# Kernel tuning notes

Measured on AMD Instinct MI355X. Metric: run time of the kernel, lower is better.

Reference implementation:

```python
import jax, jax.numpy as jnp
import numpy as np

NEG_SLOPE = 0.2  # PyG GATConv default


def gat_conv(x, src, dst, W, att_src, att_dst, bias, num_nodes, concat):
    """Faithful PyG GATConv forward (self-loops assumed already added).
    x: [N, F_in]; src/dst: [E]; W: [F_in, H*C]; att_src/att_dst: [H, C]."""
    H, C = att_src.shape
    h = (x @ W).reshape(num_nodes, H, C)                      # [N, H, C]
    a_src = (h * att_src[None]).sum(-1)                       # [N, H]
    a_dst = (h * att_dst[None]).sum(-1)                       # [N, H]
    alpha = jax.nn.leaky_relu(a_src[src] + a_dst[dst], NEG_SLOPE)  # [E, H]
    # segment softmax over incoming edges of each dst node (numerically stable)
    m = jax.ops.segment_max(alpha, dst, num_segments=num_nodes)    # [N, H]
    e = jnp.exp(alpha - m[dst])                                    # [E, H]
    denom = jax.ops.segment_sum(e, dst, num_segments=num_nodes)    # [N, H]
    w = e / jnp.maximum(denom[dst], 1e-16)                         # [E, H]
    msg = h[src] * w[:, :, None]                                   # [E, H, C]
    out = jax.ops.segment_sum(msg, dst, num_segments=num_nodes)    # [N, H, C]
    out = out.reshape(num_nodes, H * C) if concat else out.mean(axis=1)
    return out + bias


def setup_inputs() -> dict:
    key = jax.random.key(0)
    ks = jax.random.split(key, 16)
    N, E, n_drones = 100000, 1600000, 10000
    IN, HID, OUT, HEADS = 6, 64, 2, 4

    x = jax.random.normal(ks[0], (N, IN), dtype=jnp.float32)
    # first n_drones nodes are drones (x[:,5] == 1.0), rest 0.0
    x = x.at[:, 5].set((jnp.arange(N) < n_drones).astype(jnp.float32))
    edge_index = jax.random.randint(ks[1], (2, E), 0, N, dtype=jnp.int64)

    s = 0.1
    params = {
        "W1": jax.random.normal(ks[2], (IN, HEADS * HID), jnp.float32) * s,
        "att_src1": jax.random.normal(ks[3], (HEADS, HID), jnp.float32) * s,
        "att_dst1": jax.random.normal(ks[4], (HEADS, HID), jnp.float32) * s,
        "b1": jax.random.normal(ks[5], (HEADS * HID,), jnp.float32) * s,
        "W2": jax.random.normal(ks[6], (HEADS * HID, HID), jnp.float32) * s,
        "att_src2": jax.random.normal(ks[7], (1, HID), jnp.float32) * s,
        "att_dst2": jax.random.normal(ks[8], (1, HID), jnp.float32) * s,
        "b2": jax.random.normal(ks[9], (HID,), jnp.float32) * s,
        "fc1_w": jax.random.normal(ks[10], (HID, 64), jnp.float32) * s,
        "fc1_b": jax.random.normal(ks[11], (64,), jnp.float32) * s,
        "fc2_w": jax.random.normal(ks[12], (64, OUT), jnp.float32) * s,
        "fc2_b": jax.random.normal(ks[13], (OUT,), jnp.float32) * s,
    }
    return {"x": x, "edge_index": edge_index, "n_drones": n_drones, **params}


def reference(x, edge_index, n_drones, W1, att_src1, att_dst1, b1,
              W2, att_src2, att_dst2, b2, fc1_w, fc1_b, fc2_w, fc2_b):
    N = x.shape[0]
    action_scale = 2.0
    # add self loops (PyG GATConv default add_self_loops=True)
    loop = jnp.arange(N, dtype=edge_index.dtype)
    src = jnp.concatenate([edge_index[0], loop])
    dst = jnp.concatenate([edge_index[1], loop])

    h = jax.nn.elu(gat_conv(x, src, dst, W1, att_src1, att_dst1, b1, N, concat=True))
    h = jax.nn.elu(gat_conv(h, src, dst, W2, att_src2, att_dst2, b2, N, concat=False))

    drone_idx = jnp.nonzero(x[:, 5] == 1.0, size=n_drones)[0]
    h_drones = h[drone_idx]                                   # [n_drones, HID]
    out = jnp.tanh(jax.nn.relu(h_drones @ fc1_w + fc1_b) @ fc2_w + fc2_b)
    return out * action_scale
```

## Files before the change

### kernel.cpp

```cpp
#include <hip/hip_runtime.h>
#include <hip/hip_fp16.h>
#include <math.h>

#define CAP 48
#define PARTBITS 8
#define BINW 256
#define NB 240
#define SEGCAP 48

typedef float f32x4 __attribute__((ext_vector_type(4)));
typedef __bf16 bf16x8 __attribute__((ext_vector_type(8)));
typedef unsigned short ushort8 __attribute__((ext_vector_type(8)));
typedef int i32x4 __attribute__((ext_vector_type(4)));
typedef int i32x2 __attribute__((ext_vector_type(2)));

__device__ __forceinline__ float leaky(float x){ return x > 0.f ? x : 0.2f * x; }
__device__ __forceinline__ float eluf(float x){ return x > 0.f ? x : __expf(x) - 1.f; }
__device__ __forceinline__ unsigned short f2bf(float f){
  unsigned u = __float_as_uint(f);
  u += 0x7FFF + ((u >> 16) & 1);
  return (unsigned short)(u >> 16);
}
__device__ __forceinline__ float bf2f(unsigned short u){
  return __uint_as_float(((unsigned)u) << 16);
}
__device__ __forceinline__ unsigned short f2h(float f){
  return __half_as_ushort(__float2half(f));
}
__device__ __forceinline__ float h2f(unsigned short u){
  return __half2float(__ushort_as_half(u));
}

__global__ __launch_bounds__(256) void k1_att1(const float* __restrict__ x,
    const float* __restrict__ W1, const float* __restrict__ as1,
    const float* __restrict__ ad1, const float* __restrict__ W2,
    unsigned short* __restrict__ Bfrag, ushort8* __restrict__ rec8,
    int* __restrict__ gtail, int N){
  __shared__ float vw[48];
  int t = threadIdx.x;
  int gid = blockIdx.x * 256 + t;
  if (gid == 0) *gtail = 0;
  if (gid < 16384){
    int j  = gid & 7;
    int L  = (gid >> 3) & 63;
    int ct = (gid >> 9) & 3;
    int ks = gid >> 11;
    int k = ks*32 + ((L >> 4) & 3)*8 + j;
    int c = ct*16 + (L & 15);
    Bfrag[gid] = f2bf(W2[k*64 + c]);
  }
  if (t < 48){
    int side = t / 24, r = t % 24, f = r / 4, h = r % 4;
    const float* att = side ? ad1 : as1;
    float s = 0.f;
    for (int c = 0; c < 64; ++c) s += W1[f*256 + h*64 + c] * att[h*64 + c];
    vw[side*24 + f*4 + h] = s;
  }
  __syncthreads();
  int n = gid;
  if (n >= N) return;
  float xf[6];
  for (int f = 0; f < 6; ++f) xf[f] = x[n*6 + f];
  float as[4], ad[4];
  for (int h = 0; h < 4; ++h){
    float s = 0.f, d = 0.f;
    for (int f = 0; f < 6; ++f){ s += xf[f] * vw[f*4 + h]; d += xf[f] * vw[24 + f*4 + h]; }
    as[h] = s; ad[h] = d;
  }
  ushort8 v0, v1;
  v0[0]=f2bf(xf[0]); v0[1]=f2bf(xf[1]); v0[2]=f2bf(xf[2]); v0[3]=f2bf(xf[3]);
  v0[4]=f2bf(xf[4]); v0[5]=f2bf(xf[5]); v0[6]=f2h(as[0]); v0[7]=f2h(as[1]);
  v1[0]=f2h(as[2]); v1[1]=f2h(as[3]); v1[2]=f2h(ad[0]); v1[3]=f2h(ad[1]);
  v1[4]=f2h(ad[2]); v1[5]=f2h(ad[3]); v1[6]=0; v1[7]=0;
  rec8[n*2 + 0] = v0;
  rec8[n*2 + 1] = v1;
}

__global__ __launch_bounds__(256) void k2a_route(const int* __restrict__ ei,
    int E, int NR, i32x2* __restrict__ queue, int* __restrict__ qcnt){
  __shared__ int lcnt[512];
  int t = threadIdx.x, blk = blockIdx.x;
  for (int i = t; i < NR; i += 256) lcnt[i] = 0;
  __syncthreads();
  int E4 = E >> 2;
  const i32x4* s4 = (const i32x4*)ei;
  const i32x4* d4 = (const i32x4*)(ei + E);
  for (int i = blk*256 + t; i < E4; i += NB*256){
    i32x4 s = __builtin_nontemporal_load(s4 + i);
    i32x4 d = __builtin_nontemporal_load(d4 + i);
    #pragma unroll
    for (int j = 0; j < 4; ++j){
      int p = d[j] >> PARTBITS;
      int r = atomicAdd(&lcnt[p], 1);
      if (r < SEGCAP){ i32x2 v = {d[j], s[j]}; queue[((size_t)p*NB + blk)*SEGCAP + r] = v; }
    }
  }
  if (blk == 0 && t < (E & 3)){
    int e = E4*4 + t;
    int dd = ei[E + e], ss = ei[e];
    int p = dd >> PARTBITS;
    int r = atomicAdd(&lcnt[p], 1);
    if (r < SEGCAP){ i32x2 v = {dd, ss}; queue[((size_t)p*NB + blk)*SEGCAP + r] = v; }
  }
  __syncthreads();
  for (int i = t; i < NR; i += 256) qcnt[(size_t)i*NB + blk] = lcnt[i];
}

__global__ __launch_bounds__(1024) void k2b_build(const i32x2* __restrict__ queue,
    const int* __restrict__ qcnt, int* __restrict__ cnt,
    int* __restrict__ row_start, int* __restrict__ bucket,
    int* __restrict__ gtail){
  __shared__ int lc[BINW];
  __shared__ int lq[NB];
  __shared__ int spref[NB];
  __shared__ int npref[BINW+1];
  __shared__ int scan[BINW];
  __shared__ int lbuck[BINW*CAP];
  __shared__ int gbase_s;
  int t = threadIdx.x, bin = blockIdx.x;
  if (t < BINW) lc[t] = 0;
  for (int i = t; i < NB; i += 1024) lq[i] = min(qcnt[(size_t)bin*NB + i], SEGCAP);
  __syncthreads();
  if (t < 256) scan[t] = (t < NB) ? lq[t] : 0;
  __syncthreads();
  for (int off = 1; off < 256; off <<= 1){
    int v = 0;
    if (t < 256 && t >= off) v = scan[t - off];
    __syncthreads();
    if (t < 256) scan[t] += v;
    __syncthreads();
  }
  if (t < NB) spref[t] = (t == 0) ? 0 : scan[t-1];
  int V = scan[NB-1];
  __syncthreads();
  const i32x2* q = queue + (size_t)bin*NB*SEGCAP;
  for (int vi = t; vi < V; vi += 1024){
    int lo = 0, hi = NB-1;
    while (lo < hi){ int mid = (lo+hi+1) >> 1; if (spref[mid] <= vi) lo = mid; else hi = mid-1; }
    i32x2 pr = q[lo*SEGCAP + (vi - spref[lo])];
    int ld = pr.x & (BINW-1);
    int pos = atomicAdd(&lc[ld], 1);
    if (pos < CAP) lbuck[ld*CAP + pos] = pr.y;
  }
  __syncthreads();
  if (t < 256) scan[t] = min(lc[t], CAP);
  __syncthreads();
  for (int off = 1; off < 256; off <<= 1){
    int v = 0;
    if (t < 256 && t >= off) v = scan[t - off];
    __syncthreads();
    if (t < 256) scan[t] += v;
    __syncthreads();
  }
  if (t < 256) npref[t] = (t == 0) ? 0 : scan[t-1];
  if (t == 0){
    npref[BINW] = scan[BINW-1];
    gbase_s = atomicAdd(gtail, scan[BINW-1]);
  }
  __syncthreads();
  int gbase = gbase_s;
  int Vn = npref[BINW];
  for (int vi = t; vi < Vn; vi += 1024){
    int lo = 0, hi = BINW-1;
    while (lo < hi){ int mid = (lo+hi+1) >> 1; if (npref[mid] <= vi) lo = mid; else hi = mid-1; }
    bucket[gbase + vi] = lbuck[lo*CAP + (vi - npref[lo])];
  }
  if (t < BINW){
    cnt[bin*BINW + t] = min(lc[t], CAP);
    row_start[bin*BINW + t] = gbase + npref[t];
  }
}

__global__ __launch_bounds__(256) void k3_agg1(const ushort8* __restrict__ rec8,
    const int* __restrict__ cnt, const int* __restrict__ row_start,
    const int* __restrict__ bucket, float* __restrict__ aggr, int N){
  int n = blockIdx.x * 256 + threadIdx.x;
  if (n >= N) return;
  ushort8 v0 = rec8[n*2+0], v1 = rec8[n*2+1];
  float xf[6] = {bf2f(v0[0]), bf2f(v0[1]), bf2f(v0[2]), bf2f(v0[3]), bf2f(v0[4]), bf2f(v0[5])};
  float as[4] = {h2f(v0[6]), h2f(v0[7]), h2f(v1[0]), h2f(v1[1])};
  float ad[4] = {h2f(v1[2]), h2f(v1[3]), h2f(v1[4]), h2f(v1[5])};
  float acc[4][6], den[4];
  for (int h = 0; h < 4; ++h){
    float e0 = __expf(leaky(as[h] + ad[h]));
    den[h] = e0;
    for (int f = 0; f < 6; ++f) acc[h][f] = e0 * xf[f];
  }
  int deg = cnt[n];
  const int* bk = bucket + row_start[n];
  int i = 0;
  for (; i + 4 <= deg; i += 4){
    int sid[4];
    #pragma unroll
    for (int j = 0; j < 4; ++j) sid[j] = bk[i+j];
    ushort8 ra[4], rb[4];
    #pragma unroll
    for (int j = 0; j < 4; ++j){
      ra[j] = rec8[sid[j]*2+0]; rb[j] = rec8[sid[j]*2+1];
    }
    #pragma unroll
    for (int j = 0; j < 4; ++j){
      float sx[6] = {bf2f(ra[j][0]), bf2f(ra[j][1]), bf2f(ra[j][2]),
                     bf2f(ra[j][3]), bf2f(ra[j][4]), bf2f(ra[j][5])};
      float sa[4] = {h2f(ra[j][6]), h2f(ra[j][7]), h2f(rb[j][0]), h2f(rb[j][1])};
      #pragma unroll
      for (int h = 0; h < 4; ++h){
        float e = __expf(leaky(sa[h] + ad[h]));
        den[h] += e;
        #pragma unroll
        for (int f = 0; f < 6; ++f) acc[h][f] += e * sx[f];
      }
    }
  }
  for (; i < deg; ++i){
    int s = bk[i];
    ushort8 a0 = rec8[s*2+0], a1 = rec8[s*2+1];
    float sx[6] = {bf2f(a0[0]), bf2f(a0[1]), bf2f(a0[2]), bf2f(a0[3]), bf2f(a0[4]), bf2f(a0[5])};
    float sa[4] = {h2f(a0[6]), h2f(a0[7]), h2f(a1[0]), h2f(a1[1])};
    for (int h = 0; h < 4; ++h){
      float e = __expf(leaky(sa[h] + ad[h]));
      den[h] += e;
      for (int f = 0; f < 6; ++f) acc[h][f] += e * sx[f];
    }
  }
  float4* o = (float4*)(aggr + (size_t)n*32);
  o[0] = make_float4(acc[0][0], acc[0][1], acc[0][2], acc[0][3]);
  o[1] = make_float4(acc[0][4], acc[0][5], acc[1][0], acc[1][1]);
  o[2] = make_float4(acc[1][2], acc[1][3], acc[1][4], acc[1][5]);
  o[3] = make_float4(acc[2][0], acc[2][1], acc[2][2], acc[2][3]);
  o[4] = make_float4(acc[2][4], acc[2][5], acc[3][0], acc[3][1]);
  o[5] = make_float4(acc[3][2], acc[3][3], acc[3][4], acc[3][5]);
  o[6] = make_float4(den[0], den[1], den[2], den[3]);
}

__global__ __launch_bounds__(256) void k4_mfma(
    const float* __restrict__ aggr, const float* __restrict__ W1,
    const float* __restrict__ b1, const unsigned short* __restrict__ Bfrag,
    const float* __restrict__ as2v, const float* __restrict__ ad2v,
    unsigned short* __restrict__ h2h, float2* __restrict__ a2, int N){
  __shared__ float w1s[6*256];
  __shared__ float b1s[256];
  __shared__ ushort8 bfs[2048];
  int t = threadIdx.x;
  {
    const float4* w1g = (const float4*)W1;
    float4* w1l = (float4*)w1s;
    for (int i = t; i < 384; i += 256) w1l[i] = w1g[i];
    if (t < 64) ((float4*)b1s)[t] = ((const float4*)b1)[t];
    const ushort8* bfg = (const ushort8*)Bfrag;
    #pragma unroll
    for (int i = 0; i < 8; ++i) bfs[t + 256*i] = bfg[t + 256*i];
  }
  int L = t & 63;
  int w = t >> 6;
  int base = blockIdx.x * 64;
  int m = L & 15;
  int quad = L >> 4;
  int na = base + w*16 + m;
  int nc = min(na, N-1);
  const float4* A4 = (const float4*)(aggr + (size_t)nc*32);
  float4 q0=A4[0], q1=A4[1], q2=A4[2], q3=A4[3], q4=A4[4], q5=A4[5], q6=A4[6];
  float d0=1.f/q6.x, d1=1.f/q6.y, d2=1.f/q6.z, d3=1.f/q6.w;
  float af[24];
  af[0]=q0.x*d0;  af[1]=q0.y*d0;  af[2]=q0.z*d0;  af[3]=q0.w*d0;  af[4]=q1.x*d0;  af[5]=q1.y*d0;
  af[6]=q1.z*d1;  af[7]=q1.w*d1;  af[8]=q2.x*d1;  af[9]=q2.y*d1;  af[10]=q2.z*d1; af[11]=q2.w*d1;
  af[12]=q3.x*d2; af[13]=q3.y*d2; af[14]=q3.z*d2; af[15]=q3.w*d2; af[16]=q4.x*d2; af[17]=q4.y*d2;
  af[18]=q4.z*d3; af[19]=q4.w*d3; af[20]=q5.x*d3; af[21]=q5.y*d3; af[22]=q5.z*d3; af[23]=q5.w*d3;

  f32x4 acc[4];
  #pragma unroll
  for (int ct = 0; ct < 4; ++ct) acc[ct] = (f32x4){0.f, 0.f, 0.f, 0.f};
  __syncthreads();

  #pragma unroll
  for (int ks = 0; ks < 8; ++ks){
    int kb = ks*32 + quad*8;
    int kc = kb >> 6;
    const float* afk = af + kc*6;
    float4 bb0 = *(const float4*)(b1s + kb);
    float4 bb1 = *(const float4*)(b1s + kb + 4);
    float s0=bb0.x, s1=bb0.y, s2=bb0.z, s3=bb0.w;
    float s4=bb1.x, s5=bb1.y, s6=bb1.z, s7=bb1.w;
    #pragma unroll
    for (int f = 0; f < 6; ++f){
      float a = afk[f];
      float4 w0 = *(const float4*)(w1s + f*256 + kb);
      float4 w1 = *(const float4*)(w1s + f*256 + kb + 4);
      s0 += a*w0.x; s1 += a*w0.y; s2 += a*w0.z; s3 += a*w0.w;
      s4 += a*w1.x; s5 += a*w1.y; s6 += a*w1.z; s7 += a*w1.w;
    }
    ushort8 ap;
    ap[0]=f2bf(eluf(s0)); ap[1]=f2bf(eluf(s1)); ap[2]=f2bf(eluf(s2)); ap[3]=f2bf(eluf(s3));
    ap[4]=f2bf(eluf(s4)); ap[5]=f2bf(eluf(s5)); ap[6]=f2bf(eluf(s6)); ap[7]=f2bf(eluf(s7));
    bf16x8 av = __builtin_bit_cast(bf16x8, ap);
    #pragma unroll
    for (int ct = 0; ct < 4; ++ct){
      bf16x8 bv = __builtin_bit_cast(bf16x8, bfs[(ks*4 + ct)*64 + L]);
      acc[ct] = __builtin_amdgcn_mfma_f32_16x16x32_bf16(av, bv, acc[ct], 0, 0, 0);
    }
  }

  float asv[4], adv[4];
  #pragma unroll
  for (int ct = 0; ct < 4; ++ct){ asv[ct] = as2v[ct*16 + m]; adv[ct] = ad2v[ct*16 + m]; }
  float ps[4] = {0,0,0,0}, pd[4] = {0,0,0,0};
  #pragma unroll
  for (int ct = 0; ct < 4; ++ct)
    #pragma unroll
    for (int r = 0; r < 4; ++r){
      ps[r] += acc[ct][r] * asv[ct];
      pd[r] += acc[ct][r] * adv[ct];
    }
  #pragma unroll
  for (int r = 0; r < 4; ++r){
    int nr = base + w*16 + quad*4 + r;
    if (nr < N){
      #pragma unroll
      for (int ct = 0; ct < 4; ++ct)
        h2h[(size_t)nr*64 + ct*16 + m] = f2h(acc[ct][r]);
    }
  }
  #pragma unroll
  for (int mask = 1; mask <= 8; mask <<= 1){
    #pragma unroll
    for (int r = 0; r < 4; ++r){
      ps[r] += __shfl_xor(ps[r], mask, 64);
      pd[r] += __shfl_xor(pd[r], mask, 64);
    }
  }
  if (m == 0){
    #pragma unroll
    for (int r = 0; r < 4; ++r){
      int nr = base + w*16 + quad*4 + r;
      if (nr < N) a2[nr] = make_float2(ps[r], pd[r]);
    }
  }
}

__global__ __launch_bounds__(256) void k5_out(
    const unsigned short* __restrict__ h2h, const float2* __restrict__ a2,
    const int* __restrict__ cnt, const int* __restrict__ row_start,
    const int* __restrict__ bucket, const float* __restrict__ b2,
    const float* __restrict__ fc1w, const float* __restrict__ fc1b,
    const float* __restrict__ fc2w, const float* __restrict__ fc2b,
    float* __restrict__ out, int ND){
  __shared__ float hb[4][64];
  int lane = threadIdx.x & 63;
  int w = threadIdx.x >> 6;
  int n = blockIdx.x * 4 + w;
  if (n >= ND) return;
  float2 self = a2[n];
  float adv = self.y;
  float e0 = __expf(leaky(self.x + adv));
  float den = e0;
  float acc = e0 * h2f(h2h[(size_t)n*64 + lane]);
  int deg = cnt[n];
  const int* bk = bucket + row_start[n];
  int i = 0;
  for (; i + 4 <= deg; i += 4){
    int sid[4];
    #pragma unroll
    for (int j = 0; j < 4; ++j) sid[j] = bk[i+j];
    float av[4]; unsigned short hv4[4];
    #pragma unroll
    for (int j = 0; j < 4; ++j){
      av[j] = a2[sid[j]].x;
      hv4[j] = h2h[(size_t)sid[j]*64 + lane];
    }
    #pragma unroll
    for (int j = 0; j < 4; ++j){
      float e = __expf(leaky(av[j] + adv));
      den += e;
      acc += e * h2f(hv4[j]);
    }
  }
  for (; i < deg; ++i){
    int s = bk[i];
    float e = __expf(leaky(a2[s].x + adv));
    den += e;
    acc += e * h2f(h2h[(size_t)s*64 + lane]);
  }
  float hv = eluf(acc / den + b2[lane]);
  hb[w][lane] = hv;
  float t1 = fc1b[lane];
  for (int k = 0; k < 64; ++k) t1 += hb[w][k] * fc1w[k*64 + lane];
  t1 = fmaxf(t1, 0.f);
  float p0 = t1 * fc2w[lane*2 + 0];
  float p1 = t1 * fc2w[lane*2 + 1];
  for (int o = 32; o > 0; o >>= 1){
    p0 += __shfl_down(p0, o, 64);
    p1 += __shfl_down(p1, o, 64);
  }
  if (lane == 0){
    out[n*2 + 0] = tanhf(p0 + fc2b[0]) * 2.f;
    out[n*2 + 1] = tanhf(p1 + fc2b[1]) * 2.f;
  }
}

extern "C" void kernel_launch(void* const* d_in, const int* in_sizes, int n_in,
                              void* d_out, int out_size, void* d_ws, size_t ws_size,
                              hipStream_t stream){
  const float* x    = (const float*)d_in[0];
  const int*   ei   = (const int*)d_in[1];
  const float* W1   = (const float*)d_in[3];
  const float* as1  = (const float*)d_in[4];
  const float* ad1  = (const float*)d_in[5];
  const float* b1   = (const float*)d_in[6];
  const float* W2   = (const float*)d_in[7];
  const float* as2  = (const float*)d_in[8];
  const float* ad2  = (const float*)d_in[9];
  const float* b2   = (const float*)d_in[10];
  const float* fc1w = (const float*)d_in[11];
  const float* fc1b = (const float*)d_in[12];
  const float* fc2w = (const float*)d_in[13];
  const float* fc2b = (const float*)d_in[14];
  float* out = (float*)d_out;

  int N  = in_sizes[0] / 6;
  int E  = in_sizes[1] / 2;
  int ND = out_size / 2;
  int NR = (N + BINW - 1) >> PARTBITS;

  char* p = (char*)d_ws;
  auto alloc = [&](size_t bytes){ void* r = (void*)p; p += (bytes + 255) & ~(size_t)255; return r; };
  int*            cnt    = (int*)           alloc((size_t)NR * BINW * 4);
  int*            rowst  = (int*)           alloc((size_t)NR * BINW * 4);
  int*            bucket = (int*)           alloc(((size_t)E + 1024) * 4);
  ushort8*        rec8   = (ushort8*)       alloc((size_t)N * 32);
  float*          aggr   = (float*)         alloc((size_t)N * 128);
  unsigned short* h2h    = (unsigned short*)alloc((size_t)N * 128);
  float2*         a2     = (float2*)        alloc((size_t)N * 8);
  unsigned short* Bfrag  = (unsigned short*)alloc(16384 * 2);
  i32x2*          queue  = (i32x2*)         alloc((size_t)NR * NB * SEGCAP * 8);
  int*            qcnt   = (int*)           alloc((size_t)NR * NB * 4);
  int*            gtail  = (int*)           alloc(256);

  size_t needed = (size_t)(p - (char*)d_ws);
  if (needed > ws_size) return;

  k1_att1<<<(N + 255)/256, 256, 0, stream>>>(x, W1, as1, ad1, W2, Bfrag, rec8, gtail, N);
  k2a_route<<<NB, 256, 0, stream>>>(ei, E, NR, queue, qcnt);
  k2b_build<<<NR, 1024, 0, stream>>>(queue, qcnt, cnt, rowst, bucket, gtail);
  k3_agg1<<<(N + 255)/256, 256, 0, stream>>>(rec8, cnt, rowst, bucket, aggr, N);
  k4_mfma<<<(N + 63)/64, 256, 0, stream>>>(aggr, W1, b1, Bfrag, as2, ad2, h2h, a2, N);
  k5_out<<<(ND + 3)/4, 256, 0, stream>>>(h2h, a2, cnt, rowst, bucket, b2,
                                         fc1w, fc1b, fc2w, fc2b, out, ND);
}
```

Baseline: 194.4 us.

## Fuse route with att1, split layer-1 aggregation per head pair, fp16 normalized output

Merges the node-attention kernel and the edge-routing kernel into one launch, with a block-index split so both run concurrently. Layer-1 aggregation now uses two threads per node, each handling two heads. Each thread reads a 16-byte per-head-pair record (features plus two source scores) rather than a 32-byte record, and destination scores move to a separate small array. The aggregation normalizes by the denominator in-kernel and writes fp16 results (48 B/node instead of 128 B fp32), which cuts traffic into the MFMA kernel at some precision cost. Layer-2 attention scores are stored as separate src/dst arrays so the gather loads only the needed 4 bytes.

```diff
diff --git a/kernel.cpp b/kernel.cpp
--- a/kernel.cpp
+++ b/kernel.cpp
@@ -11,6 +11,7 @@
 typedef float f32x4 __attribute__((ext_vector_type(4)));
 typedef __bf16 bf16x8 __attribute__((ext_vector_type(8)));
 typedef unsigned short ushort8 __attribute__((ext_vector_type(8)));
+typedef unsigned short ushort4v __attribute__((ext_vector_type(4)));
 typedef int i32x4 __attribute__((ext_vector_type(4)));
 typedef int i32x2 __attribute__((ext_vector_type(2)));
 
@@ -31,79 +32,82 @@
   return __half2float(__ushort_as_half(u));
 }
 
-__global__ __launch_bounds__(256) void k1_att1(const float* __restrict__ x,
+__global__ __launch_bounds__(256) void k12a(const float* __restrict__ x,
     const float* __restrict__ W1, const float* __restrict__ as1,
     const float* __restrict__ ad1, const float* __restrict__ W2,
-    unsigned short* __restrict__ Bfrag, ushort8* __restrict__ rec8,
-    int* __restrict__ gtail, int N){
+    unsigned short* __restrict__ Bfrag, ushort8* __restrict__ recA,
+    ushort8* __restrict__ recB, ushort4v* __restrict__ recC,
+    int* __restrict__ gtail, int N, int nbk1,
+    const int* __restrict__ ei, int E, int NR,
+    i32x2* __restrict__ queue, int* __restrict__ qcnt){
   __shared__ float vw[48];
+  __shared__ int lcnt[512];
   int t = threadIdx.x;
-  int gid = blockIdx.x * 256 + t;
-  if (gid == 0) *gtail = 0;
-  if (gid < 16384){
-    int j  = gid & 7;
-    int L  = (gid >> 3) & 63;
-    int ct = (gid >> 9) & 3;
-    int ks = gid >> 11;
-    int k = ks*32 + ((L >> 4) & 3)*8 + j;
-    int c = ct*16 + (L & 15);
-    Bfrag[gid] = f2bf(W2[k*64 + c]);
-  }
-  if (t < 48){
-    int side = t / 24, r = t % 24, f = r / 4, h = r % 4;
-    const float* att = side ? ad1 : as1;
-    float s = 0.f;
-    for (int c = 0; c < 64; ++c) s += W1[f*256 + h*64 + c] * att[h*64 + c];
-    vw[side*24 + f*4 + h] = s;
-  }
-  __syncthreads();
-  int n = gid;
-  if (n >= N) return;
-  float xf[6];
-  for (int f = 0; f < 6; ++f) xf[f] = x[n*6 + f];
-  float as[4], ad[4];
-  for (int h = 0; h < 4; ++h){
-    float s = 0.f, d = 0.f;
-    for (int f = 0; f < 6; ++f){ s += xf[f] * vw[f*4 + h]; d += xf[f] * vw[24 + f*4 + h]; }
-    as[h] = s; ad[h] = d;
-  }
-  ushort8 v0, v1;
-  v0[0]=f2bf(xf[0]); v0[1]=f2bf(xf[1]); v0[2]=f2bf(xf[2]); v0[3]=f2bf(xf[3]);
-  v0[4]=f2bf(xf[4]); v0[5]=f2bf(xf[5]); v0[6]=f2h(as[0]); v0[7]=f2h(as[1]);
-  v1[0]=f2h(as[2]); v1[1]=f2h(as[3]); v1[2]=f2h(ad[0]); v1[3]=f2h(ad[1]);
-  v1[4]=f2h(ad[2]); v1[5]=f2h(ad[3]); v1[6]=0; v1[7]=0;
-  rec8[n*2 + 0] = v0;
-  rec8[n*2 + 1] = v1;
-}
-
-__global__ __launch_bounds__(256) void k2a_route(const int* __restrict__ ei,
-    int E, int NR, i32x2* __restrict__ queue, int* __restrict__ qcnt){
-  __shared__ int lcnt[512];
-  int t = threadIdx.x, blk = blockIdx.x;
-  for (int i = t; i < NR; i += 256) lcnt[i] = 0;
-  __syncthreads();
-  int E4 = E >> 2;
-  const i32x4* s4 = (const i32x4*)ei;
-  const i32x4* d4 = (const i32x4*)(ei + E);
-  for (int i = blk*256 + t; i < E4; i += NB*256){
-    i32x4 s = __builtin_nontemporal_load(s4 + i);
-    i32x4 d = __builtin_nontemporal_load(d4 + i);
-    #pragma unroll
-    for (int j = 0; j < 4; ++j){
-      int p = d[j] >> PARTBITS;
+  if ((int)blockIdx.x < nbk1){
+    int gid = blockIdx.x * 256 + t;
+    if (gid == 0) *gtail = 0;
+    if (gid < 16384){
+      int j  = gid & 7;
+      int L  = (gid >> 3) & 63;
+      int ct = (gid >> 9) & 3;
+      int ks = gid >> 11;
+      int k = ks*32 + ((L >> 4) & 3)*8 + j;
+      int c = ct*16 + (L & 15);
+      Bfrag[gid] = f2bf(W2[k*64 + c]);
+    }
+    if (t < 48){
+      int side = t / 24, r = t % 24, f = r / 4, h = r % 4;
+      const float* att = side ? ad1 : as1;
+      float s = 0.f;
+      for (int c = 0; c < 64; ++c) s += W1[f*256 + h*64 + c] * att[h*64 + c];
+      vw[side*24 + f*4 + h] = s;
+    }
+    __syncthreads();
+    int n = gid;
+    if (n >= N) return;
+    float xf[6];
+    for (int f = 0; f < 6; ++f) xf[f] = x[n*6 + f];
+    float as[4], ad[4];
+    for (int h = 0; h < 4; ++h){
+      float s = 0.f, d = 0.f;
+      for (int f = 0; f < 6; ++f){ s += xf[f] * vw[f*4 + h]; d += xf[f] * vw[24 + f*4 + h]; }
+      as[h] = s; ad[h] = d;
+    }
+    ushort8 va, vb;
+    va[0]=f2bf(xf[0]); va[1]=f2bf(xf[1]); va[2]=f2bf(xf[2]); va[3]=f2bf(xf[3]);
+    va[4]=f2bf(xf[4]); va[5]=f2bf(xf[5]); va[6]=f2h(as[0]); va[7]=f2h(as[1]);
+    vb = va; vb[6]=f2h(as[2]); vb[7]=f2h(as[3]);
+    ushort4v vc = {f2h(ad[0]), f2h(ad[1]), f2h(ad[2]), f2h(ad[3])};
+    recA[n] = va;
+    recB[n] = vb;
+    recC[n] = vc;
+  } else {
+    int blk = blockIdx.x - nbk1;
+    for (int i = t; i < NR; i += 256) lcnt[i] = 0;
+    __syncthreads();
+    int E4 = E >> 2;
+    const i32x4* s4 = (const i32x4*)ei;
+    const i32x4* d4 = (const i32x4*)(ei + E);
+    for (int i = blk*256 + t; i < E4; i += NB*256){
+      i32x4 s = __builtin_nontemporal_load(s4 + i);
+      i32x4 d = __builtin_nontemporal_load(d4 + i);
+      #pragma unroll
+      for (int j = 0; j < 4; ++j){
+        int p = d[j] >> PARTBITS;
+        int r = atomicAdd(&lcnt[p], 1);
+        if (r < SEGCAP){ i32x2 v = {d[j], s[j]}; queue[((size_t)p*NB + blk)*SEGCAP + r] = v; }
+      }
+    }
+    if (blk == 0 && t < (E & 3)){
+      int e = E4*4 + t;
+      int dd = ei[E + e], ss = ei[e];
+      int p = dd >> PARTBITS;
       int r = atomicAdd(&lcnt[p], 1);
-      if (r < SEGCAP){ i32x2 v = {d[j], s[j]}; queue[((size_t)p*NB + blk)*SEGCAP + r] = v; }
-    }
-  }
-  if (blk == 0 && t < (E & 3)){
-    int e = E4*4 + t;
-    int dd = ei[E + e], ss = ei[e];
-    int p = dd >> PARTBITS;
-    int r = atomicAdd(&lcnt[p], 1);
-    if (r < SEGCAP){ i32x2 v = {dd, ss}; queue[((size_t)p*NB + blk)*SEGCAP + r] = v; }
-  }
-  __syncthreads();
-  for (int i = t; i < NR; i += 256) qcnt[(size_t)i*NB + blk] = lcnt[i];
+      if (r < SEGCAP){ i32x2 v = {dd, ss}; queue[((size_t)p*NB + blk)*SEGCAP + r] = v; }
+    }
+    __syncthreads();
+    for (int i = t; i < NR; i += 256) qcnt[(size_t)i*NB + blk] = lcnt[i];
+  }
 }
 
 __global__ __launch_bounds__(1024) void k2b_build(const i32x2* __restrict__ queue,
@@ -171,19 +175,25 @@
   }
 }
 
-__global__ __launch_bounds__(256) void k3_agg1(const ushort8* __restrict__ rec8,
+__global__ __launch_bounds__(256) void k3_agg1(const ushort8* __restrict__ recA,
+    const ushort8* __restrict__ recB, const ushort4v* __restrict__ recC,
     const int* __restrict__ cnt, const int* __restrict__ row_start,
-    const int* __restrict__ bucket, float* __restrict__ aggr, int N){
-  int n = blockIdx.x * 256 + threadIdx.x;
+    const int* __restrict__ bucket, ushort4v* __restrict__ afh, int N){
+  int t2 = blockIdx.x * 256 + threadIdx.x;
+  int n = t2 >> 1, hp = t2 & 1;
   if (n >= N) return;
-  ushort8 v0 = rec8[n*2+0], v1 = rec8[n*2+1];
+  const ushort8* R = hp ? recB : recA;
+  ushort8 v0 = R[n];
   float xf[6] = {bf2f(v0[0]), bf2f(v0[1]), bf2f(v0[2]), bf2f(v0[3]), bf2f(v0[4]), bf2f(v0[5])};
-  float as[4] = {h2f(v0[6]), h2f(v0[7]), h2f(v1[0]), h2f(v1[1])};
-  float ad[4] = {h2f(v1[2]), h2f(v1[3]), h2f(v1[4]), h2f(v1[5])};
-  float acc[4][6], den[4];
-  for (int h = 0; h < 4; ++h){
-    float e0 = __expf(leaky(as[h] + ad[h]));
+  float a_s[2] = {h2f(v0[6]), h2f(v0[7])};
+  ushort4v cc = recC[n];
+  float a_d[2] = {h2f(cc[hp*2]), h2f(cc[hp*2+1])};
+  float acc[2][6], den[2];
+  #pragma unroll
+  for (int h = 0; h < 2; ++h){
+    float e0 = __expf(leaky(a_s[h] + a_d[h]));
     den[h] = e0;
+    #pragma unroll
     for (int f = 0; f < 6; ++f) acc[h][f] = e0 * xf[f];
   }
   int deg = cnt[n];
@@ -193,19 +203,17 @@
     int sid[4];
     #pragma unroll
     for (int j = 0; j < 4; ++j) sid[j] = bk[i+j];
-    ushort8 ra[4], rb[4];
+    ushort8 r[4];
+    #pragma unroll
+    for (int j = 0; j < 4; ++j) r[j] = R[sid[j]];
     #pragma unroll
     for (int j = 0; j < 4; ++j){
-      ra[j] = rec8[sid[j]*2+0]; rb[j] = rec8[sid[j]*2+1];
-    }
-    #pragma unroll
-    for (int j = 0; j < 4; ++j){
-      float sx[6] = {bf2f(ra[j][0]), bf2f(ra[j][1]), bf2f(ra[j][2]),
-                     bf2f(ra[j][3]), bf2f(ra[j][4]), bf2f(ra[j][5])};
-      float sa[4] = {h2f(ra[j][6]), h2f(ra[j][7]), h2f(rb[j][0]), h2f(rb[j][1])};
+      float sx[6] = {bf2f(r[j][0]), bf2f(r[j][1]), bf2f(r[j][2]),
+                     bf2f(r[j][3]), bf2f(r[j][4]), bf2f(r[j][5])};
+      float sa[2] = {h2f(r[j][6]), h2f(r[j][7])};
       #pragma unroll
-      for (int h = 0; h < 4; ++h){
-        float e = __expf(leaky(sa[h] + ad[h]));
+      for (int h = 0; h < 2; ++h){
+        float e = __expf(leaky(sa[h] + a_d[h]));
         den[h] += e;
         #pragma unroll
         for (int f = 0; f < 6; ++f) acc[h][f] += e * sx[f];
@@ -213,31 +221,33 @@
     }
   }
   for (; i < deg; ++i){
-    int s = bk[i];
-    ushort8 a0 = rec8[s*2+0], a1 = rec8[s*2+1];
-    float sx[6] = {bf2f(a0[0]), bf2f(a0[1]), bf2f(a0[2]), bf2f(a0[3]), bf2f(a0[4]), bf2f(a0[5])};
-    float sa[4] = {h2f(a0[6]), h2f(a0[7]), h2f(a1[0]), h2f(a1[1])};
-    for (int h = 0; h < 4; ++h){
-      float e = __expf(leaky(sa[h] + ad[h]));
+    ushort8 r = R[bk[i]];
+    float sx[6] = {bf2f(r[0]), bf2f(r[1]), bf2f(r[2]), bf2f(r[3]), bf2f(r[4]), bf2f(r[5])};
+    float sa[2] = {h2f(r[6]), h2f(r[7])};
+    #pragma unroll
+    for (int h = 0; h < 2; ++h){
+      float e = __expf(leaky(sa[h] + a_d[h]));
       den[h] += e;
+      #pragma unroll
       for (int f = 0; f < 6; ++f) acc[h][f] += e * sx[f];
     }
   }
-  float4* o = (float4*)(aggr + (size_t)n*32);
-  o[0] = make_float4(acc[0][0], acc[0][1], acc[0][2], acc[0][3]);
-  o[1] = make_float4(acc[0][4], acc[0][5], acc[1][0], acc[1][1]);
-  o[2] = make_float4(acc[1][2], acc[1][3], acc[1][4], acc[1][5]);
-  o[3] = make_float4(acc[2][0], acc[2][1], acc[2][2], acc[2][3]);
-  o[4] = make_float4(acc[2][4], acc[2][5], acc[3][0], acc[3][1]);
-  o[5] = make_float4(acc[3][2], acc[3][3], acc[3][4], acc[3][5]);
-  o[6] = make_float4(den[0], den[1], den[2], den[3]);
+  float d0 = 1.f / den[0], d1 = 1.f / den[1];
+  ushort4v o0 = {f2h(acc[0][0]*d0), f2h(acc[0][1]*d0), f2h(acc[0][2]*d0), f2h(acc[0][3]*d0)};
+  ushort4v o1 = {f2h(acc[0][4]*d0), f2h(acc[0][5]*d0), f2h(acc[1][0]*d1), f2h(acc[1][1]*d1)};
+  ushort4v o2 = {f2h(acc[1][2]*d1), f2h(acc[1][3]*d1), f2h(acc[1][4]*d1), f2h(acc[1][5]*d1)};
+  size_t ob = (size_t)n*6 + hp*3;
+  afh[ob + 0] = o0;
+  afh[ob + 1] = o1;
+  afh[ob + 2] = o2;
 }
 
 __global__ __launch_bounds__(256) void k4_mfma(
-    const float* __restrict__ aggr, const float* __restrict__ W1,
+    const ushort4v* __restrict__ afh, const float* __restrict__ W1,
     const float* __restrict__ b1, const unsigned short* __restrict__ Bfrag,
     const float* __restrict__ as2v, const float* __restrict__ ad2v,
-    unsigned short* __restrict__ h2h, float2* __restrict__ a2, int N){
+    unsigned short* __restrict__ h2h, float* __restrict__ a2s,
+    float* __restrict__ a2d, int N){
   __shared__ float w1s[6*256];
   __shared__ float b1s[256];
   __shared__ ushort8 bfs[2048];
@@ -258,15 +268,17 @@
   int quad = L >> 4;
   int na = base + w*16 + m;
   int nc = min(na, N-1);
-  const float4* A4 = (const float4*)(aggr + (size_t)nc*32);
-  float4 q0=A4[0], q1=A4[1], q2=A4[2], q3=A4[3], q4=A4[4], q5=A4[5], q6=A4[6];
-  float d0=1.f/q6.x, d1=1.f/q6.y, d2=1.f/q6.z, d3=1.f/q6.w;
   float af[24];
-  af[0]=q0.x*d0;  af[1]=q0.y*d0;  af[2]=q0.z*d0;  af[3]=q0.w*d0;  af[4]=q1.x*d0;  af[5]=q1.y*d0;
-  af[6]=q1.z*d1;  af[7]=q1.w*d1;  af[8]=q2.x*d1;  af[9]=q2.y*d1;  af[10]=q2.z*d1; af[11]=q2.w*d1;
-  af[12]=q3.x*d2; af[13]=q3.y*d2; af[14]=q3.z*d2; af[15]=q3.w*d2; af[16]=q4.x*d2; af[17]=q4.y*d2;
-  af[18]=q4.z*d3; af[19]=q4.w*d3; af[20]=q5.x*d3; af[21]=q5.y*d3; af[22]=q5.z*d3; af[23]=q5.w*d3;
-
+  {
+    const ushort8* A8 = (const ushort8*)(afh + (size_t)nc*6);
+    ushort8 u0 = A8[0], u1 = A8[1], u2 = A8[2];
+    #pragma unroll
+    for (int j = 0; j < 8; ++j) af[j] = h2f(u0[j]);
+    #pragma unroll
+    for (int j = 0; j < 8; ++j) af[8+j] = h2f(u1[j]);
+    #pragma unroll
+    for (int j = 0; j < 8; ++j) af[16+j] = h2f(u2[j]);
+  }
   f32x4 acc[4];
   #pragma unroll
   for (int ct = 0; ct < 4; ++ct) acc[ct] = (f32x4){0.f, 0.f, 0.f, 0.f};
@@ -332,26 +344,25 @@
     #pragma unroll
     for (int r = 0; r < 4; ++r){
       int nr = base + w*16 + quad*4 + r;
-      if (nr < N) a2[nr] = make_float2(ps[r], pd[r]);
+      if (nr < N){ a2s[nr] = ps[r]; a2d[nr] = pd[r]; }
     }
   }
 }
 
 __global__ __launch_bounds__(256) void k5_out(
-    const unsigned short* __restrict__ h2h, const float2* __restrict__ a2,
-    const int* __restrict__ cnt, const int* __restrict__ row_start,
-    const int* __restrict__ bucket, const float* __restrict__ b2,
-    const float* __restrict__ fc1w, const float* __restrict__ fc1b,
-    const float* __restrict__ fc2w, const float* __restrict__ fc2b,
-    float* __restrict__ out, int ND){
+    const unsigned short* __restrict__ h2h, const float* __restrict__ a2s,
+    const float* __restrict__ a2d, const int* __restrict__ cnt,
+    const int* __restrict__ row_start, const int* __restrict__ bucket,
+    const float* __restrict__ b2, const float* __restrict__ fc1w,
+    const float* __restrict__ fc1b, const float* __restrict__ fc2w,
+    const float* __restrict__ fc2b, float* __restrict__ out, int ND){
   __shared__ float hb[4][64];
   int lane = threadIdx.x & 63;
   int w = threadIdx.x >> 6;
   int n = blockIdx.x * 4 + w;
   if (n >= ND) return;
-  float2 self = a2[n];
-  float adv = self.y;
-  float e0 = __expf(leaky(self.x + adv));
+  float adv = a2d[n];
+  float e0 = __expf(leaky(a2s[n] + adv));
   float den = e0;
   float acc = e0 * h2f(h2h[(size_t)n*64 + lane]);
   int deg = cnt[n];
@@ -364,7 +375,7 @@
     float av[4]; unsigned short hv4[4];
     #pragma unroll
     for (int j = 0; j < 4; ++j){
-      av[j] = a2[sid[j]].x;
+      av[j] = a2s[sid[j]];
       hv4[j] = h2h[(size_t)sid[j]*64 + lane];
     }
     #pragma unroll
@@ -376,7 +387,7 @@
   }
   for (; i < deg; ++i){
     int s = bk[i];
-    float e = __expf(leaky(a2[s].x + adv));
+    float e = __expf(leaky(a2s[s] + adv));
     den += e;
     acc += e * h2f(h2h[(size_t)s*64 + lane]);
   }
@@ -420,16 +431,20 @@
   int E  = in_sizes[1] / 2;
   int ND = out_size / 2;
   int NR = (N + BINW - 1) >> PARTBITS;
+  int nbk1 = (N + 255) / 256;
 
   char* p = (char*)d_ws;
   auto alloc = [&](size_t bytes){ void* r = (void*)p; p += (bytes + 255) & ~(size_t)255; return r; };
   int*            cnt    = (int*)           alloc((size_t)NR * BINW * 4);
   int*            rowst  = (int*)           alloc((size_t)NR * BINW * 4);
   int*            bucket = (int*)           alloc(((size_t)E + 1024) * 4);
-  ushort8*        rec8   = (ushort8*)       alloc((size_t)N * 32);
-  float*          aggr   = (float*)         alloc((size_t)N * 128);
+  ushort8*        recA   = (ushort8*)       alloc((size_t)N * 16);
+  ushort8*        recB   = (ushort8*)       alloc((size_t)N * 16);
+  ushort4v*       recC   = (ushort4v*)      alloc((size_t)N * 8);
+  ushort4v*       afh    = (ushort4v*)      alloc((size_t)N * 48);
   unsigned short* h2h    = (unsigned short*)alloc((size_t)N * 128);
-  float2*         a2     = (float2*)        alloc((size_t)N * 8);
+  float*          a2s    = (float*)         alloc((size_t)N * 4);
+  float*          a2d    = (float*)         alloc((size_t)N * 4);
   unsigned short* Bfrag  = (unsigned short*)alloc(16384 * 2);
   i32x2*          queue  = (i32x2*)         alloc((size_t)NR * NB * SEGCAP * 8);
   int*            qcnt   = (int*)           alloc((size_t)NR * NB * 4);
@@ -438,11 +453,13 @@
   size_t needed = (size_t)(p - (char*)d_ws);
   if (needed > ws_size) return;
 
-  k1_att1<<<(N + 255)/256, 256, 0, stream>>>(x, W1, as1, ad1, W2, Bfrag, rec8, gtail, N);
-  k2a_route<<<NB, 256, 0, stream>>>(ei, E, NR, queue, qcnt);
+  k12a<<<nbk1 + NB, 256, 0, stream>>>(x, W1, as1, ad1, W2, Bfrag, recA, recB,
+                                      recC, gtail, N, nbk1, ei, E, NR, queue, qcnt);
   k2b_build<<<NR, 1024, 0, stream>>>(queue, qcnt, cnt, rowst, bucket, gtail);
-  k3_agg1<<<(N + 255)/256, 256, 0, stream>>>(rec8, cnt, rowst, bucket, aggr, N);
-  k4_mfma<<<(N + 63)/64, 256, 0, stream>>>(aggr, W1, b1, Bfrag, as2, ad2, h2h, a2, N);
-  k5_out<<<(ND + 3)/4, 256, 0, stream>>>(h2h, a2, cnt, rowst, bucket, b2,
+  k3_agg1<<<(2*N + 255)/256, 256, 0, stream>>>(recA, recB, recC, cnt, rowst,
+                                               bucket, afh, N);
+  k4_mfma<<<(N + 63)/64, 256, 0, stream>>>(afh, W1, b1, Bfrag, as2, ad2,
+                                           h2h, a2s, a2d, N);
+  k5_out<<<(ND + 3)/4, 256, 0, stream>>>(h2h, a2s, a2d, cnt, rowst, bucket, b2,
                                          fc1w, fc1b, fc2w, fc2b, out, ND);
 }
```

New measurement: 192.0 us. Within noise of the previous version (-1.2%).
